# Kernel tuning notes

Hardware: AMD Instinct MI355X
Metric: run time of the kernel (lower is better)

The kernel has to match this reference:

```python
import jax, jax.numpy as jnp
import numpy as np

N = 50000      # nodes
E = 800000     # edges (before self-loops)
F_IN = 256     # nfeat
HEADS = 8      # nhead
C1 = 16        # hidden_sizes (per-head channels of conv1)
NCLS = 40      # nclass
NEG_SLOPE = 0.2


def setup_inputs() -> dict:
    key = jax.random.key(0)
    ks = jax.random.split(key, 12)
    s = 0.1
    x = jax.random.normal(ks[0], (N, F_IN), dtype=jnp.float32)
    edge_index = jax.random.randint(ks[1], (2, E), 0, N, dtype=jnp.int64)
    edge_attr = jax.random.normal(ks[2], (E,), dtype=jnp.float32)  # unused by forward
    W1 = jax.random.normal(ks[3], (F_IN, HEADS * C1), dtype=jnp.float32) * s
    att_src1 = jax.random.normal(ks[4], (HEADS, C1), dtype=jnp.float32) * s
    att_dst1 = jax.random.normal(ks[5], (HEADS, C1), dtype=jnp.float32) * s
    b1 = jnp.zeros((HEADS * C1,), dtype=jnp.float32)
    W2 = jax.random.normal(ks[6], (HEADS * C1, NCLS), dtype=jnp.float32) * s
    att_src2 = jax.random.normal(ks[7], (1, NCLS), dtype=jnp.float32) * s
    att_dst2 = jax.random.normal(ks[8], (1, NCLS), dtype=jnp.float32) * s
    b2 = jnp.zeros((NCLS,), dtype=jnp.float32)
    return {"x": x, "edge_index": edge_index, "edge_attr": edge_attr,
            "W1": W1, "att_src1": att_src1, "att_dst1": att_dst1, "b1": b1,
            "W2": W2, "att_src2": att_src2, "att_dst2": att_dst2, "b2": b2}


def gat_layer(x, W, att_src, att_dst, bias, src, dst, concat):
    """PyG-style GATConv (eval mode, no dropout). src/dst include self-loops."""
    H, C = att_src.shape
    h = (x @ W).reshape(-1, H, C)                     # [N,H,C]
    a_src = (h * att_src[None]).sum(-1)               # [N,H]
    a_dst = (h * att_dst[None]).sum(-1)               # [N,H]
    e = jax.nn.leaky_relu(a_src[src] + a_dst[dst], NEG_SLOPE)  # [Etot,H]
    # segment softmax over destination neighborhoods
    m = jax.ops.segment_max(e, dst, num_segments=N)   # [N,H]
    m = jax.lax.stop_gradient(jnp.where(jnp.isfinite(m), m, 0.0))
    p = jnp.exp(e - m[dst])
    denom = jax.ops.segment_sum(p, dst, num_segments=N)
    alpha = p / (denom[dst] + 1e-16)                  # [Etot,H]
    out = jax.ops.segment_sum(alpha[:, :, None] * h[src], dst, num_segments=N)  # [N,H,C]
    out = out.reshape(-1, H * C) if concat else out.mean(axis=1)
    return out + bias


def reference(x, edge_index, edge_attr, W1, att_src1, att_dst1, b1, W2, att_src2, att_dst2, b2):
    # add self loops (PyG GATConv default)
    loops = jnp.arange(N, dtype=edge_index.dtype)
    src = jnp.concatenate([edge_index[0], loops])
    dst = jnp.concatenate([edge_index[1], loops])
    # eval mode: F.dropout is identity
    h = jax.nn.elu(gat_layer(x, W1, att_src1, att_dst1, b1, src, dst, concat=True))
    final = gat_layer(h, W2, att_src2, att_dst2, b2, src, dst, concat=False)
    return final, jax.nn.log_softmax(final, axis=1)
```

## Files before the change

### kernel.cpp

```cpp
#include <hip/hip_runtime.h>

#define NN 50000
#define EE 800000
#define FIN 256
#define HD 8
#define C1 16
#define HC 128
#define NC 40
#define NEG 0.2f
#define CAP 64
#define BM 64
#define BM2 64
#define GB1 ((NN + BM - 1) / BM)
#define NP_N (NN / 8)
#define SCB 2048
#define PREPB 19

typedef __attribute__((ext_vector_type(8))) short short8;
typedef __attribute__((ext_vector_type(4))) float f32x4;
union FragU { uint4 u; short8 s; };

__device__ __forceinline__ float leaky(float v){ return v > 0.f ? v : NEG * v; }

__device__ __forceinline__ unsigned int f2bf(float f){
  unsigned int u = __float_as_uint(f);
  u += 0x7fffu + ((u >> 16) & 1u);
  return u >> 16;
}
__device__ __forceinline__ unsigned int pack2bf(float a, float b){
  return f2bf(a) | (f2bf(b) << 16);
}
__device__ __forceinline__ float bflo(unsigned int u){ return __uint_as_float(u << 16); }
__device__ __forceinline__ float bfhi(unsigned int u){ return __uint_as_float(u & 0xffff0000u); }
__device__ __forceinline__ float bfus(unsigned short u){ return __uint_as_float((unsigned int)u << 16); }

__device__ __forceinline__ void gld_lds16(const void* g, void* l){
  __builtin_amdgcn_global_load_lds((const __attribute__((address_space(1))) unsigned int*)g,
                                   (__attribute__((address_space(3))) unsigned int*)l,
                                   16, 0, 0);
}

__global__ __launch_bounds__(256) void k_prep(const float* __restrict__ W1,
                                              uint4* __restrict__ W1bfs,
                                              const float* __restrict__ W2,
                                              uint4* __restrict__ W2bfs,
                                              const int* __restrict__ ei,
                                              int* __restrict__ cnt,
                                              int* __restrict__ srcp){
  const int tid = threadIdx.x;
  if (blockIdx.x < 16){
    int f = blockIdx.x * 256 + tid;
    int lane = f & 63, nt = (f >> 6) & 7, kt = f >> 9;
    int quad = lane >> 4, l16 = lane & 15;
    const float* src = W1 + (size_t)(kt * 32 + quad * 8) * HC + nt * 16 + l16;
    unsigned int p[4];
#pragma unroll
    for (int jj = 0; jj < 4; jj++)
      p[jj] = pack2bf(src[(size_t)(2 * jj) * HC], src[(size_t)(2 * jj + 1) * HC]);
    W1bfs[f] = make_uint4(p[0], p[1], p[2], p[3]);
    return;
  }
  if (blockIdx.x < PREPB){
    int f = (blockIdx.x - 16) * 256 + tid;
    int lane = f & 63, frag = f >> 6;
    int kt = frag / 3, nt = frag - kt * 3;
    int quad = lane >> 4, l16 = lane & 15;
    int n = nt * 16 + l16;
    int k0 = kt * 32 + quad * 8;
    unsigned int p[4];
#pragma unroll
    for (int jj = 0; jj < 4; jj++){
      float v0 = (n < NC) ? W2[(size_t)(k0 + 2 * jj) * NC + n] : 0.f;
      float v1 = (n < NC) ? W2[(size_t)(k0 + 2 * jj + 1) * NC + n] : 0.f;
      p[jj] = pack2bf(v0, v1);
    }
    W2bfs[f] = make_uint4(p[0], p[1], p[2], p[3]);
    return;
  }
  const int b = blockIdx.x - PREPB;
  const int part = b & 7, rank = b >> 3;
  const int lo = part * NP_N, hi = lo + NP_N;
  for (int e = rank * 256 + tid; e < EE; e += 256 * 256){
    int d = ei[EE + e];
    if (d >= lo && d < hi){
      int s = ei[e];
      int pos = atomicAdd(&cnt[d], 1);
      if (pos < CAP) srcp[d * CAP + pos] = s;
    }
  }
}

__global__ __launch_bounds__(256, 2) void k_gemm1(const float* __restrict__ x,
                                                  const uint4* __restrict__ W1bfs,
                                                  const float* __restrict__ att_s,
                                                  const float* __restrict__ att_d,
                                                  unsigned short* __restrict__ h1b,
                                                  float* __restrict__ as1,
                                                  float* __restrict__ ad1){
  __shared__ float xs[BM * FIN];
  const int tid = threadIdx.x;
  const int wave = tid >> 6, lane = tid & 63;
  const int quad = lane >> 4, l16 = lane & 15;
  const int m0 = blockIdx.x * BM;
  const int wr0 = wave * 16;

#pragma unroll
  for (int i = 0; i < 16; i++){
    int grow = m0 + wr0 + i; if (grow >= NN) grow = NN - 1;
    const float* src = x + (size_t)grow * FIN + ((lane ^ (i & 7)) << 2);
    gld_lds16(src, &xs[(wr0 + i) * FIN]);
  }

  FragU bf[8];
#pragma unroll
  for (int nt = 0; nt < 8; nt++) bf[nt].u = W1bfs[nt * 64 + lane];

  asm volatile("s_waitcnt vmcnt(0)" ::: "memory");
  __builtin_amdgcn_sched_barrier(0);

  f32x4 acc[8];
#pragma unroll
  for (int t = 0; t < 8; t++) acc[t] = (f32x4){0.f, 0.f, 0.f, 0.f};

  const int swz = l16 & 7;
  const float* xrow = &xs[(wr0 + l16) * FIN];
#pragma unroll
  for (int kt = 0; kt < 8; kt++){
    FragU bn[8];
    if (kt < 7){
#pragma unroll
      for (int nt = 0; nt < 8; nt++)
        bn[nt].u = W1bfs[((kt + 1) * 8 + nt) * 64 + lane];
    }
    const int g0 = kt * 8 + quad * 2;
    const float4 a0 = *(const float4*)(xrow + ((g0 ^ swz) << 2));
    const float4 a1 = *(const float4*)(xrow + (((g0 + 1) ^ swz) << 2));
    FragU af;
    af.u = make_uint4(pack2bf(a0.x, a0.y), pack2bf(a0.z, a0.w),
                      pack2bf(a1.x, a1.y), pack2bf(a1.z, a1.w));
#pragma unroll
    for (int nt = 0; nt < 8; nt++)
      acc[nt] = __builtin_amdgcn_mfma_f32_16x16x32_bf16(af.s, bf[nt].s, acc[nt], 0, 0, 0);
    if (kt < 7){
#pragma unroll
      for (int nt = 0; nt < 8; nt++) bf[nt] = bn[nt];
    }
  }

  float sv[8], dv[8];
#pragma unroll
  for (int h = 0; h < 8; h++){ sv[h] = att_s[h * 16 + l16]; dv[h] = att_d[h * 16 + l16]; }
#pragma unroll
  for (int r = 0; r < 4; r++){
    const int gr = m0 + wr0 + quad * 4 + r;
    float s[8], d[8];
#pragma unroll
    for (int h = 0; h < 8; h++){ s[h] = acc[h][r] * sv[h]; d[h] = acc[h][r] * dv[h]; }
#pragma unroll
    for (int o = 1; o < 16; o <<= 1){
#pragma unroll
      for (int h = 0; h < 8; h++){ s[h] += __shfl_xor(s[h], o); d[h] += __shfl_xor(d[h], o); }
    }
    if (gr < NN){
#pragma unroll
      for (int h = 0; h < 8; h++)
        h1b[(size_t)gr * HC + h * 16 + l16] = (unsigned short)f2bf(acc[h][r]);
      if (l16 == 0){
        *(float4*)(as1 + gr * 8)     = make_float4(s[0], s[1], s[2], s[3]);
        *(float4*)(as1 + gr * 8 + 4) = make_float4(s[4], s[5], s[6], s[7]);
        *(float4*)(ad1 + gr * 8)     = make_float4(d[0], d[1], d[2], d[3]);
        *(float4*)(ad1 + gr * 8 + 4) = make_float4(d[4], d[5], d[6], d[7]);
      }
    }
  }
}

__global__ __launch_bounds__(512) void k_agg1(const int* __restrict__ srcp,
                                              const int* __restrict__ cnt,
                                              const float* __restrict__ as1,
                                              const float* __restrict__ ad1,
                                              const unsigned short* __restrict__ h1b,
                                              const float* __restrict__ b1,
                                              unsigned short* __restrict__ h2b){
  __shared__ float wls[8][64][8];
  __shared__ int   sls[8][64];
  const int lane = threadIdx.x & 63, w = threadIdx.x >> 6;
  const int n = blockIdx.x * 8 + w;
  int deg = cnt[n]; if (deg > CAP - 1) deg = CAP - 1;
  const int nE = deg + 1;
  int sA = n;
  if (lane < deg) sA = srcp[n * CAP + lane];
  sls[w][lane] = sA << 6;

  const int h = lane >> 3, e8 = lane & 7;
  const float adg = ad1[n * 8 + h];
  int nCh = (nE + 7) >> 3; if (nCh < 2) nCh = 2;

  float mx = -3.0e38f;
  for (int c = 0; c < nCh; c++){
    const int i = c * 8 + e8;
    const int s8 = sls[w][i] >> 3;
    const float v = (i < nE) ? leaky(as1[(size_t)(unsigned)(s8 + h)] + adg) : -3.0e38f;
    wls[w][i][h] = v;
    mx = fmaxf(mx, v);
  }
  mx = fmaxf(mx, __shfl_xor(mx, 1));
  mx = fmaxf(mx, __shfl_xor(mx, 2));
  mx = fmaxf(mx, __shfl_xor(mx, 4));

  float den = 0.f;
  for (int c = 0; c < nCh; c++){
    const int i = c * 8 + e8;
    const float v = wls[w][i][h];
    const float wt = (i < nE) ? __expf(v - mx) : 0.f;
    wls[w][i][h] = wt;
    den += wt;
  }
  den += __shfl_xor(den, 1);
  den += __shfl_xor(den, 2);
  den += __shfl_xor(den, 4);

  const unsigned int* hp = (const unsigned int*)h1b;
  float ax = 0.f, ay = 0.f;
  {
    unsigned int u[16]; float q[16];
#pragma unroll
    for (int i = 0; i < 16; i++){
      u[i] = hp[(size_t)(unsigned)(sls[w][i] + lane)];
      q[i] = wls[w][i][h];
    }
#pragma unroll
    for (int i = 0; i < 16; i++){ ax += q[i] * bflo(u[i]); ay += q[i] * bfhi(u[i]); }
  }
  for (int i0 = 16; i0 < nE; i0 += 8){
    unsigned int uu[8]; float qq[8];
#pragma unroll
    for (int t = 0; t < 8; t++){
      const int j = i0 + t;
      uu[t] = hp[(size_t)(unsigned)(sls[w][j] + lane)];
      qq[t] = (j < nE) ? wls[w][j][h] : 0.f;
    }
#pragma unroll
    for (int t = 0; t < 8; t++){ ax += qq[t] * bflo(uu[t]); ay += qq[t] * bfhi(uu[t]); }
  }

  const float invd = 1.f / (den + 1e-16f);
  const float2 bb = *(const float2*)(b1 + 2 * lane);
  float ox = ax * invd + bb.x;
  float oy = ay * invd + bb.y;
  ox = ox > 0.f ? ox : (__expf(ox) - 1.f);
  oy = oy > 0.f ? oy : (__expf(oy) - 1.f);
  *(unsigned int*)(h2b + (size_t)n * HC + 2 * lane) = pack2bf(ox, oy);
}

__global__ __launch_bounds__(256, 3) void k_gemm2(const unsigned short* __restrict__ h2b,
                                                  const uint4* __restrict__ W2bfs,
                                                  const float* __restrict__ att_s2,
                                                  const float* __restrict__ att_d2,
                                                  unsigned short* __restrict__ gb,
                                                  float* __restrict__ as2,
                                                  float* __restrict__ ad2){
  __shared__ unsigned short h2s[BM2 * HC];
  const int tid = threadIdx.x;
  const int wave = tid >> 6, lane = tid & 63;
  const int quad = lane >> 4, l16 = lane & 15;
  const int m0 = blockIdx.x * BM2;
  const int wr0 = wave * 16;

#pragma unroll
  for (int i = 0; i < 4; i++){
    const int rl = i * 4 + (lane >> 4);
    int grow = m0 + wr0 + rl; if (grow >= NN) grow = NN - 1;
    const int g = lane & 15;
    const unsigned short* src = h2b + (size_t)grow * HC + ((g ^ (rl & 7)) << 3);
    gld_lds16(src, &h2s[(wr0 + i * 4) * HC]);
  }

  FragU b2f[12];
#pragma unroll
  for (int f = 0; f < 12; f++) b2f[f].u = W2bfs[f * 64 + lane];

  asm volatile("s_waitcnt vmcnt(0)" ::: "memory");
  __builtin_amdgcn_sched_barrier(0);

  f32x4 acc[3];
#pragma unroll
  for (int t = 0; t < 3; t++) acc[t] = (f32x4){0.f, 0.f, 0.f, 0.f};

  const int swz = l16 & 7;
  const unsigned short* hrow = &h2s[(wr0 + l16) * HC];
#pragma unroll
  for (int kt = 0; kt < 4; kt++){
    FragU af;
    af.u = *(const uint4*)(hrow + (((kt * 4 + quad) ^ swz) << 3));
#pragma unroll
    for (int nt = 0; nt < 3; nt++)
      acc[nt] = __builtin_amdgcn_mfma_f32_16x16x32_bf16(af.s, b2f[kt * 3 + nt].s, acc[nt], 0, 0, 0);
  }

  float sv[3], dv[3];
#pragma unroll
  for (int nt = 0; nt < 3; nt++){
    const int c = nt * 16 + l16;
    sv[nt] = (c < NC) ? att_s2[c] : 0.f;
    dv[nt] = (c < NC) ? att_d2[c] : 0.f;
  }
#pragma unroll
  for (int r = 0; r < 4; r++){
    const int gr = m0 + wr0 + quad * 4 + r;
    float s = acc[0][r] * sv[0] + acc[1][r] * sv[1] + acc[2][r] * sv[2];
    float d = acc[0][r] * dv[0] + acc[1][r] * dv[1] + acc[2][r] * dv[2];
#pragma unroll
    for (int o = 1; o < 16; o <<= 1){ s += __shfl_xor(s, o); d += __shfl_xor(d, o); }
    if (gr < NN){
#pragma unroll
      for (int nt = 0; nt < 3; nt++){
        const int c = nt * 16 + l16;
        if (c < NC) gb[(size_t)gr * NC + c] = (unsigned short)f2bf(acc[nt][r]);
      }
      if (l16 == 0){ as2[gr] = s; ad2[gr] = d; }
    }
  }
}

__global__ __launch_bounds__(512) void k_agg2(const int* __restrict__ srcp,
                                              const int* __restrict__ cnt,
                                              const float* __restrict__ as2,
                                              const float* __restrict__ ad2,
                                              const unsigned short* __restrict__ gb,
                                              const float* __restrict__ b2,
                                              float* __restrict__ out){
  __shared__ float wls[8][64];
  __shared__ int   sls[8][64];
  const int lane = threadIdx.x & 63, w = threadIdx.x >> 6;
  const int n = blockIdx.x * 8 + w;
  int deg = cnt[n]; if (deg > CAP - 1) deg = CAP - 1;
  const int nE = deg + 1;
  const bool act = (lane <= deg);
  int sA = n;
  if (lane < deg) sA = srcp[n * CAP + lane];
  const float ad = ad2[n];
  float v = act ? leaky(as2[sA] + ad) : -3.0e38f;
  sls[w][lane] = sA * NC;
  float mx = v;
#pragma unroll
  for (int o = 1; o < 64; o <<= 1) mx = fmaxf(mx, __shfl_xor(mx, o));
  float wt = act ? __expf(v - mx) : 0.f;
  float den = wt;
#pragma unroll
  for (int o = 1; o < 64; o <<= 1) den += __shfl_xor(den, o);
  wls[w][lane] = wt;

  const int c = min(lane, NC - 1);
  float acc = 0.f;
  {
    float g[16], q[16];
#pragma unroll
    for (int i = 0; i < 16; i++){
      g[i] = bfus(gb[(size_t)(unsigned)(sls[w][i] + c)]);
      q[i] = wls[w][i];
    }
#pragma unroll
    for (int i = 0; i < 16; i++) acc += q[i] * g[i];
  }
  for (int i0 = 16; i0 < nE; i0 += 8){
    float gg[8], qq[8];
#pragma unroll
    for (int t = 0; t < 8; t++){
      const int j = i0 + t;
      gg[t] = bfus(gb[(size_t)(unsigned)(sls[w][j] + c)]);
      qq[t] = wls[w][j];
    }
#pragma unroll
    for (int t = 0; t < 8; t++) acc += qq[t] * gg[t];
  }
  const float invd = 1.f / (den + 1e-16f);
  const bool cl = (lane < NC);
  float f = acc * invd + b2[c];
  if (cl) out[(size_t)n * NC + lane] = f;
  float fv = cl ? f : -3.4e38f;
  float m2 = fv;
#pragma unroll
  for (int o = 1; o < 64; o <<= 1) m2 = fmaxf(m2, __shfl_xor(m2, o));
  float ex = cl ? __expf(fv - m2) : 0.f;
#pragma unroll
  for (int o = 1; o < 64; o <<= 1) ex += __shfl_xor(ex, o);
  const float lse = m2 + __logf(ex);
  if (cl) out[(size_t)(NN * NC) + (size_t)n * NC + lane] = fv - lse;
}

extern "C" void kernel_launch(void* const* d_in, const int* in_sizes, int n_in,
                              void* d_out, int out_size, void* d_ws, size_t ws_size,
                              hipStream_t stream){
  const float* x      = (const float*)d_in[0];
  const int*   ei     = (const int*)  d_in[1];
  const float* W1     = (const float*)d_in[3];
  const float* att_s1 = (const float*)d_in[4];
  const float* att_d1 = (const float*)d_in[5];
  const float* b1     = (const float*)d_in[6];
  const float* W2     = (const float*)d_in[7];
  const float* att_s2 = (const float*)d_in[8];
  const float* att_d2 = (const float*)d_in[9];
  const float* b2     = (const float*)d_in[10];
  float* out = (float*)d_out;

  char* wp = (char*)d_ws;
  uint4* W1bfs = (uint4*)wp;                 wp += (size_t)4096 * 16;
  uint4* W2bfs = (uint4*)wp;                 wp += (size_t)768 * 16;
  unsigned short* h1b = (unsigned short*)wp; wp += (size_t)NN * HC * 2;
  unsigned short* h2b = (unsigned short*)wp; wp += (size_t)NN * HC * 2;
  unsigned short* gb  = (unsigned short*)wp; wp += (size_t)NN * NC * 2;
  float* as1 = (float*)wp;                   wp += (size_t)NN * HD * 4;
  float* ad1 = (float*)wp;                   wp += (size_t)NN * HD * 4;
  float* as2 = (float*)wp;                   wp += (size_t)NN * 4;
  float* ad2 = (float*)wp;                   wp += (size_t)NN * 4;
  int* cnt   = (int*)wp;                     wp += (size_t)NN * 4;
  int* srcp  = (int*)wp;                     wp += (size_t)NN * CAP * 4;

  hipMemsetAsync(cnt, 0, (size_t)NN * sizeof(int), stream);
  k_prep  <<<PREPB + SCB, 256, 0, stream>>>(W1, W1bfs, W2, W2bfs, ei, cnt, srcp);
  k_gemm1 <<<GB1, 256, 0, stream>>>(x, W1bfs, att_s1, att_d1, h1b, as1, ad1);
  k_agg1  <<<NN / 8, 512, 0, stream>>>(srcp, cnt, as1, ad1, h1b, b1, h2b);
  k_gemm2 <<<(NN + BM2 - 1) / BM2, 256, 0, stream>>>(h2b, W2bfs, att_s2, att_d2, gb, as2, ad2);
  k_agg2  <<<NN / 8, 512, 0, stream>>>(srcp, cnt, as2, ad2, gb, b2, out);
}
```

Before: 238.2 us.

## Pre-convert x to bf16 in prep and process two nodes per wave in agg1

Adds blocks to the prep kernel that convert x to bf16 into workspace, so the first GEMM loads half-width rows into LDS and can run at higher occupancy. A fallback fp32 GEMM is kept for when the workspace is too small. The layer-1 aggregation now handles two destination nodes per wave with 32 lanes each loading 4 channels. This adds an extra full pass over x (read fp32, write bf16), and wave-level loops follow the larger of the two degrees.

```diff
diff --git a/kernel.cpp b/kernel.cpp
--- a/kernel.cpp
+++ b/kernel.cpp
@@ -15,6 +15,7 @@
 #define NP_N (NN / 8)
 #define SCB 2048
 #define PREPB 19
+#define CONVB 1024
 
 typedef __attribute__((ext_vector_type(8))) short short8;
 typedef __attribute__((ext_vector_type(4))) float f32x4;
@@ -44,6 +45,9 @@
                                               uint4* __restrict__ W1bfs,
                                               const float* __restrict__ W2,
                                               uint4* __restrict__ W2bfs,
+                                              const float* __restrict__ x,
+                                              uint4* __restrict__ xb,
+                                              int convb,
                                               const int* __restrict__ ei,
                                               int* __restrict__ cnt,
                                               int* __restrict__ srcp){
@@ -77,7 +81,18 @@
     W2bfs[f] = make_uint4(p[0], p[1], p[2], p[3]);
     return;
   }
-  const int b = blockIdx.x - PREPB;
+  if (blockIdx.x < PREPB + convb){
+    const int cb = blockIdx.x - PREPB;
+    const int stride = convb * 256;
+    for (int idx = cb * 256 + tid; idx < NN * FIN / 8; idx += stride){
+      const float4 v0 = *(const float4*)(x + (size_t)idx * 8);
+      const float4 v1 = *(const float4*)(x + (size_t)idx * 8 + 4);
+      xb[idx] = make_uint4(pack2bf(v0.x, v0.y), pack2bf(v0.z, v0.w),
+                           pack2bf(v1.x, v1.y), pack2bf(v1.z, v1.w));
+    }
+    return;
+  }
+  const int b = blockIdx.x - PREPB - convb;
   const int part = b & 7, rank = b >> 3;
   const int lo = part * NP_N, hi = lo + NP_N;
   for (int e = rank * 256 + tid; e < EE; e += 256 * 256){
@@ -90,14 +105,14 @@
   }
 }
 
-__global__ __launch_bounds__(256, 2) void k_gemm1(const float* __restrict__ x,
-                                                  const uint4* __restrict__ W1bfs,
-                                                  const float* __restrict__ att_s,
-                                                  const float* __restrict__ att_d,
-                                                  unsigned short* __restrict__ h1b,
-                                                  float* __restrict__ as1,
-                                                  float* __restrict__ ad1){
-  __shared__ float xs[BM * FIN];
+__global__ __launch_bounds__(256, 4) void k_gemm1b(const unsigned short* __restrict__ xb,
+                                                   const uint4* __restrict__ W1bfs,
+                                                   const float* __restrict__ att_s,
+                                                   const float* __restrict__ att_d,
+                                                   unsigned short* __restrict__ h1b,
+                                                   float* __restrict__ as1,
+                                                   float* __restrict__ ad1){
+  __shared__ unsigned short xs[BM * FIN];
   const int tid = threadIdx.x;
   const int wave = tid >> 6, lane = tid & 63;
   const int quad = lane >> 4, l16 = lane & 15;
@@ -105,10 +120,12 @@
   const int wr0 = wave * 16;
 
 #pragma unroll
-  for (int i = 0; i < 16; i++){
-    int grow = m0 + wr0 + i; if (grow >= NN) grow = NN - 1;
-    const float* src = x + (size_t)grow * FIN + ((lane ^ (i & 7)) << 2);
-    gld_lds16(src, &xs[(wr0 + i) * FIN]);
+  for (int i = 0; i < 8; i++){
+    const int rl = wr0 + i * 2 + (lane >> 5);
+    int grow = m0 + rl; if (grow >= NN) grow = NN - 1;
+    const int g = lane & 31;
+    const unsigned short* src = xb + (size_t)grow * FIN + ((g ^ (rl & 7)) << 3);
+    gld_lds16(src, &xs[(wr0 + i * 2) * FIN]);
   }
 
   FragU bf[8];
@@ -123,7 +140,7 @@
   for (int t = 0; t < 8; t++) acc[t] = (f32x4){0.f, 0.f, 0.f, 0.f};
 
   const int swz = l16 & 7;
-  const float* xrow = &xs[(wr0 + l16) * FIN];
+  const unsigned short* xrow = &xs[(wr0 + l16) * FIN];
 #pragma unroll
   for (int kt = 0; kt < 8; kt++){
     FragU bn[8];
@@ -132,12 +149,8 @@
       for (int nt = 0; nt < 8; nt++)
         bn[nt].u = W1bfs[((kt + 1) * 8 + nt) * 64 + lane];
     }
-    const int g0 = kt * 8 + quad * 2;
-    const float4 a0 = *(const float4*)(xrow + ((g0 ^ swz) << 2));
-    const float4 a1 = *(const float4*)(xrow + (((g0 + 1) ^ swz) << 2));
     FragU af;
-    af.u = make_uint4(pack2bf(a0.x, a0.y), pack2bf(a0.z, a0.w),
-                      pack2bf(a1.x, a1.y), pack2bf(a1.z, a1.w));
+    af.u = *(const uint4*)(xrow + (((kt * 4 + quad) ^ swz) << 3));
 #pragma unroll
     for (int nt = 0; nt < 8; nt++)
       acc[nt] = __builtin_amdgcn_mfma_f32_16x16x32_bf16(af.s, bf[nt].s, acc[nt], 0, 0, 0);
@@ -175,82 +188,187 @@
   }
 }
 
-__global__ __launch_bounds__(512) void k_agg1(const int* __restrict__ srcp,
+__global__ __launch_bounds__(256, 2) void k_gemm1f(const float* __restrict__ x,
+                                                   const uint4* __restrict__ W1bfs,
+                                                   const float* __restrict__ att_s,
+                                                   const float* __restrict__ att_d,
+                                                   unsigned short* __restrict__ h1b,
+                                                   float* __restrict__ as1,
+                                                   float* __restrict__ ad1){
+  __shared__ float xs[BM * FIN];
+  const int tid = threadIdx.x;
+  const int wave = tid >> 6, lane = tid & 63;
+  const int quad = lane >> 4, l16 = lane & 15;
+  const int m0 = blockIdx.x * BM;
+  const int wr0 = wave * 16;
+#pragma unroll
+  for (int i = 0; i < 16; i++){
+    int grow = m0 + wr0 + i; if (grow >= NN) grow = NN - 1;
+    const float* src = x + (size_t)grow * FIN + ((lane ^ (i & 7)) << 2);
+    gld_lds16(src, &xs[(wr0 + i) * FIN]);
+  }
+  FragU bf[8];
+#pragma unroll
+  for (int nt = 0; nt < 8; nt++) bf[nt].u = W1bfs[nt * 64 + lane];
+  asm volatile("s_waitcnt vmcnt(0)" ::: "memory");
+  __builtin_amdgcn_sched_barrier(0);
+  f32x4 acc[8];
+#pragma unroll
+  for (int t = 0; t < 8; t++) acc[t] = (f32x4){0.f, 0.f, 0.f, 0.f};
+  const int swz = l16 & 7;
+  const float* xrow = &xs[(wr0 + l16) * FIN];
+#pragma unroll
+  for (int kt = 0; kt < 8; kt++){
+    FragU bn[8];
+    if (kt < 7){
+#pragma unroll
+      for (int nt = 0; nt < 8; nt++)
+        bn[nt].u = W1bfs[((kt + 1) * 8 + nt) * 64 + lane];
+    }
+    const int g0 = kt * 8 + quad * 2;
+    const float4 a0 = *(const float4*)(xrow + ((g0 ^ swz) << 2));
+    const float4 a1 = *(const float4*)(xrow + (((g0 + 1) ^ swz) << 2));
+    FragU af;
+    af.u = make_uint4(pack2bf(a0.x, a0.y), pack2bf(a0.z, a0.w),
+                      pack2bf(a1.x, a1.y), pack2bf(a1.z, a1.w));
+#pragma unroll
+    for (int nt = 0; nt < 8; nt++)
+      acc[nt] = __builtin_amdgcn_mfma_f32_16x16x32_bf16(af.s, bf[nt].s, acc[nt], 0, 0, 0);
+    if (kt < 7){
+#pragma unroll
+      for (int nt = 0; nt < 8; nt++) bf[nt] = bn[nt];
+    }
+  }
+  float sv[8], dv[8];
+#pragma unroll
+  for (int h = 0; h < 8; h++){ sv[h] = att_s[h * 16 + l16]; dv[h] = att_d[h * 16 + l16]; }
+#pragma unroll
+  for (int r = 0; r < 4; r++){
+    const int gr = m0 + wr0 + quad * 4 + r;
+    float s[8], d[8];
+#pragma unroll
+    for (int h = 0; h < 8; h++){ s[h] = acc[h][r] * sv[h]; d[h] = acc[h][r] * dv[h]; }
+#pragma unroll
+    for (int o = 1; o < 16; o <<= 1){
+#pragma unroll
+      for (int h = 0; h < 8; h++){ s[h] += __shfl_xor(s[h], o); d[h] += __shfl_xor(d[h], o); }
+    }
+    if (gr < NN){
+#pragma unroll
+      for (int h = 0; h < 8; h++)
+        h1b[(size_t)gr * HC + h * 16 + l16] = (unsigned short)f2bf(acc[h][r]);
+      if (l16 == 0){
+        *(float4*)(as1 + gr * 8)     = make_float4(s[0], s[1], s[2], s[3]);
+        *(float4*)(as1 + gr * 8 + 4) = make_float4(s[4], s[5], s[6], s[7]);
+        *(float4*)(ad1 + gr * 8)     = make_float4(d[0], d[1], d[2], d[3]);
+        *(float4*)(ad1 + gr * 8 + 4) = make_float4(d[4], d[5], d[6], d[7]);
+      }
+    }
+  }
+}
+
+__global__ __launch_bounds__(256) void k_agg1(const int* __restrict__ srcp,
                                               const int* __restrict__ cnt,
                                               const float* __restrict__ as1,
                                               const float* __restrict__ ad1,
                                               const unsigned short* __restrict__ h1b,
                                               const float* __restrict__ b1,
                                               unsigned short* __restrict__ h2b){
-  __shared__ float wls[8][64][8];
-  __shared__ int   sls[8][64];
+  __shared__ float wls[4][2][64][8];
+  __shared__ int   sls[4][2][64];
+  __shared__ float dls[4][2][8];
   const int lane = threadIdx.x & 63, w = threadIdx.x >> 6;
-  const int n = blockIdx.x * 8 + w;
-  int deg = cnt[n]; if (deg > CAP - 1) deg = CAP - 1;
-  const int nE = deg + 1;
-  int sA = n;
-  if (lane < deg) sA = srcp[n * CAP + lane];
-  sls[w][lane] = sA << 6;
-
+  const int nb = blockIdx.x * 8 + w * 2;
   const int h = lane >> 3, e8 = lane & 7;
-  const float adg = ad1[n * 8 + h];
-  int nCh = (nE + 7) >> 3; if (nCh < 2) nCh = 2;
-
-  float mx = -3.0e38f;
-  for (int c = 0; c < nCh; c++){
-    const int i = c * 8 + e8;
-    const int s8 = sls[w][i] >> 3;
-    const float v = (i < nE) ? leaky(as1[(size_t)(unsigned)(s8 + h)] + adg) : -3.0e38f;
-    wls[w][i][h] = v;
-    mx = fmaxf(mx, v);
-  }
-  mx = fmaxf(mx, __shfl_xor(mx, 1));
-  mx = fmaxf(mx, __shfl_xor(mx, 2));
-  mx = fmaxf(mx, __shfl_xor(mx, 4));
-
-  float den = 0.f;
-  for (int c = 0; c < nCh; c++){
-    const int i = c * 8 + e8;
-    const float v = wls[w][i][h];
-    const float wt = (i < nE) ? __expf(v - mx) : 0.f;
-    wls[w][i][h] = wt;
-    den += wt;
-  }
-  den += __shfl_xor(den, 1);
-  den += __shfl_xor(den, 2);
-  den += __shfl_xor(den, 4);
-
-  const unsigned int* hp = (const unsigned int*)h1b;
-  float ax = 0.f, ay = 0.f;
+
+  int degs[2], nEs[2];
+#pragma unroll
+  for (int j = 0; j < 2; j++){
+    int d = cnt[nb + j]; if (d > CAP - 1) d = CAP - 1;
+    degs[j] = d; nEs[j] = d + 1;
+  }
+  const int nEm = max(nEs[0], nEs[1]);
+  int nCh = (nEm + 7) >> 3; if (nCh < 2) nCh = 2;
+
+#pragma unroll
+  for (int j = 0; j < 2; j++){
+    const int n = nb + j;
+    const int deg = degs[j], nE = nEs[j];
+    int sA = n;
+    if (lane < deg) sA = srcp[n * CAP + lane];
+    sls[w][j][lane] = sA << 5;
+
+    const float adg = ad1[n * 8 + h];
+    float mx = -3.0e38f;
+    for (int c = 0; c < nCh; c++){
+      const int i = c * 8 + e8;
+      const int s8 = sls[w][j][i] >> 2;
+      const float v = (i < nE) ? leaky(as1[(size_t)(unsigned)(s8 + h)] + adg) : -3.0e38f;
+      wls[w][j][i][h] = v;
+      mx = fmaxf(mx, v);
+    }
+    mx = fmaxf(mx, __shfl_xor(mx, 1));
+    mx = fmaxf(mx, __shfl_xor(mx, 2));
+    mx = fmaxf(mx, __shfl_xor(mx, 4));
+
+    float den = 0.f;
+    for (int c = 0; c < nCh; c++){
+      const int i = c * 8 + e8;
+      const float v = wls[w][j][i][h];
+      const float wt = (i < nE) ? __expf(v - mx) : 0.f;
+      wls[w][j][i][h] = wt;
+      den += wt;
+    }
+    den += __shfl_xor(den, 1);
+    den += __shfl_xor(den, 2);
+    den += __shfl_xor(den, 4);
+    if (e8 == 0) dls[w][j][h] = den;
+  }
+
+  const int j = lane >> 5, l32 = lane & 31, hb = l32 >> 2;
+  const uint2* hp = (const uint2*)h1b;
+  float a0 = 0.f, a1 = 0.f, a2 = 0.f, a3 = 0.f;
   {
-    unsigned int u[16]; float q[16];
+    uint2 u[16]; float q[16];
 #pragma unroll
     for (int i = 0; i < 16; i++){
-      u[i] = hp[(size_t)(unsigned)(sls[w][i] + lane)];
-      q[i] = wls[w][i][h];
-    }
-#pragma unroll
-    for (int i = 0; i < 16; i++){ ax += q[i] * bflo(u[i]); ay += q[i] * bfhi(u[i]); }
-  }
-  for (int i0 = 16; i0 < nE; i0 += 8){
-    unsigned int uu[8]; float qq[8];
+      u[i] = hp[(size_t)(unsigned)(sls[w][j][i] + l32)];
+      q[i] = wls[w][j][i][hb];
+    }
+#pragma unroll
+    for (int i = 0; i < 16; i++){
+      a0 += q[i] * bflo(u[i].x); a1 += q[i] * bfhi(u[i].x);
+      a2 += q[i] * bflo(u[i].y); a3 += q[i] * bfhi(u[i].y);
+    }
+  }
+  for (int i0 = 16; i0 < nEm; i0 += 8){
+    uint2 uu[8]; float qq[8];
 #pragma unroll
     for (int t = 0; t < 8; t++){
-      const int j = i0 + t;
-      uu[t] = hp[(size_t)(unsigned)(sls[w][j] + lane)];
-      qq[t] = (j < nE) ? wls[w][j][h] : 0.f;
-    }
-#pragma unroll
-    for (int t = 0; t < 8; t++){ ax += qq[t] * bflo(uu[t]); ay += qq[t] * bfhi(uu[t]); }
-  }
-
-  const float invd = 1.f / (den + 1e-16f);
-  const float2 bb = *(const float2*)(b1 + 2 * lane);
-  float ox = ax * invd + bb.x;
-  float oy = ay * invd + bb.y;
-  ox = ox > 0.f ? ox : (__expf(ox) - 1.f);
-  oy = oy > 0.f ? oy : (__expf(oy) - 1.f);
-  *(unsigned int*)(h2b + (size_t)n * HC + 2 * lane) = pack2bf(ox, oy);
+      const int i = i0 + t;
+      uu[t] = hp[(size_t)(unsigned)(sls[w][j][i] + l32)];
+      qq[t] = wls[w][j][i][hb];
+    }
+#pragma unroll
+    for (int t = 0; t < 8; t++){
+      a0 += qq[t] * bflo(uu[t].x); a1 += qq[t] * bfhi(uu[t].x);
+      a2 += qq[t] * bflo(uu[t].y); a3 += qq[t] * bfhi(uu[t].y);
+    }
+  }
+
+  const int n = nb + j;
+  const float invd = 1.f / (dls[w][j][hb] + 1e-16f);
+  const float4 bb = *(const float4*)(b1 + 4 * l32);
+  float o0 = a0 * invd + bb.x;
+  float o1 = a1 * invd + bb.y;
+  float o2 = a2 * invd + bb.z;
+  float o3 = a3 * invd + bb.w;
+  o0 = o0 > 0.f ? o0 : (__expf(o0) - 1.f);
+  o1 = o1 > 0.f ? o1 : (__expf(o1) - 1.f);
+  o2 = o2 > 0.f ? o2 : (__expf(o2) - 1.f);
+  o3 = o3 > 0.f ? o3 : (__expf(o3) - 1.f);
+  uint2 pk; pk.x = pack2bf(o0, o1); pk.y = pack2bf(o2, o3);
+  ((uint2*)h2b)[(size_t)n * 32 + l32] = pk;
 }
 
 __global__ __launch_bounds__(256, 3) void k_gemm2(const unsigned short* __restrict__ h2b,
@@ -416,11 +534,20 @@
   float* ad2 = (float*)wp;                   wp += (size_t)NN * 4;
   int* cnt   = (int*)wp;                     wp += (size_t)NN * 4;
   int* srcp  = (int*)wp;                     wp += (size_t)NN * CAP * 4;
+  uint4* xb  = (uint4*)wp;                   wp += (size_t)NN * FIN * 2;
+
+  const bool usebf = ws_size >= (size_t)(wp - (char*)d_ws);
+  const int convb = usebf ? CONVB : 0;
 
   hipMemsetAsync(cnt, 0, (size_t)NN * sizeof(int), stream);
-  k_prep  <<<PREPB + SCB, 256, 0, stream>>>(W1, W1bfs, W2, W2bfs, ei, cnt, srcp);
-  k_gemm1 <<<GB1, 256, 0, stream>>>(x, W1bfs, att_s1, att_d1, h1b, as1, ad1);
-  k_agg1  <<<NN / 8, 512, 0, stream>>>(srcp, cnt, as1, ad1, h1b, b1, h2b);
+  k_prep <<<PREPB + convb + SCB, 256, 0, stream>>>(W1, W1bfs, W2, W2bfs, x, xb, convb,
+                                                   ei, cnt, srcp);
+  if (usebf)
+    k_gemm1b <<<GB1, 256, 0, stream>>>((const unsigned short*)xb, W1bfs, att_s1, att_d1,
+                                       h1b, as1, ad1);
+  else
+    k_gemm1f <<<GB1, 256, 0, stream>>>(x, W1bfs, att_s1, att_d1, h1b, as1, ad1);
+  k_agg1  <<<NN / 8, 256, 0, stream>>>(srcp, cnt, as1, ad1, h1b, b1, h2b);
   k_gemm2 <<<(NN + BM2 - 1) / BM2, 256, 0, stream>>>(h2b, W2bfs, att_s2, att_d2, gb, as2, ad2);
   k_agg2  <<<NN / 8, 512, 0, stream>>>(srcp, cnt, as2, ad2, gb, b2, out);
 }
```

Result: no change. 240.4 us (+0.9%).

## Process two nodes per wave in agg1 with 8-byte gathers; vectorize edge scatter

Applied to the files above, without the earlier changes.

The first-layer aggregation now has each 64-lane wave handle two destination nodes. Each half-wave gathers 8-byte rows (four bf16 channels per lane) instead of 4-byte pairs, and the block shrinks to 256 threads. This is meant to halve the number of waves and use wider memory transactions for the neighbour feature gather. The cost is that each wave loops to the larger of the two node degrees, so some lanes idle. Separately, the edge-scatter prep blocks are moved to the front of the grid and read destination indices two at a time as int2.

```diff
diff --git a/kernel.cpp b/kernel.cpp
--- a/kernel.cpp
+++ b/kernel.cpp
@@ -48,8 +48,28 @@
                                               int* __restrict__ cnt,
                                               int* __restrict__ srcp){
   const int tid = threadIdx.x;
-  if (blockIdx.x < 16){
-    int f = blockIdx.x * 256 + tid;
+  if (blockIdx.x < SCB){
+    const int part = blockIdx.x & 7, rank = blockIdx.x >> 3;
+    const int lo = part * NP_N, hi = lo + NP_N;
+    const int2* dp = (const int2*)(ei + EE);
+    for (int e2 = rank * 256 + tid; e2 < EE / 2; e2 += 256 * 256){
+      const int2 d2 = dp[e2];
+      if (d2.x >= lo && d2.x < hi){
+        int s = ei[2 * e2];
+        int pos = atomicAdd(&cnt[d2.x], 1);
+        if (pos < CAP) srcp[d2.x * CAP + pos] = s;
+      }
+      if (d2.y >= lo && d2.y < hi){
+        int s = ei[2 * e2 + 1];
+        int pos = atomicAdd(&cnt[d2.y], 1);
+        if (pos < CAP) srcp[d2.y * CAP + pos] = s;
+      }
+    }
+    return;
+  }
+  const int pb = blockIdx.x - SCB;
+  if (pb < 16){
+    int f = pb * 256 + tid;
     int lane = f & 63, nt = (f >> 6) & 7, kt = f >> 9;
     int quad = lane >> 4, l16 = lane & 15;
     const float* src = W1 + (size_t)(kt * 32 + quad * 8) * HC + nt * 16 + l16;
@@ -60,34 +80,20 @@
     W1bfs[f] = make_uint4(p[0], p[1], p[2], p[3]);
     return;
   }
-  if (blockIdx.x < PREPB){
-    int f = (blockIdx.x - 16) * 256 + tid;
-    int lane = f & 63, frag = f >> 6;
-    int kt = frag / 3, nt = frag - kt * 3;
-    int quad = lane >> 4, l16 = lane & 15;
-    int n = nt * 16 + l16;
-    int k0 = kt * 32 + quad * 8;
-    unsigned int p[4];
-#pragma unroll
-    for (int jj = 0; jj < 4; jj++){
-      float v0 = (n < NC) ? W2[(size_t)(k0 + 2 * jj) * NC + n] : 0.f;
-      float v1 = (n < NC) ? W2[(size_t)(k0 + 2 * jj + 1) * NC + n] : 0.f;
-      p[jj] = pack2bf(v0, v1);
-    }
-    W2bfs[f] = make_uint4(p[0], p[1], p[2], p[3]);
-    return;
-  }
-  const int b = blockIdx.x - PREPB;
-  const int part = b & 7, rank = b >> 3;
-  const int lo = part * NP_N, hi = lo + NP_N;
-  for (int e = rank * 256 + tid; e < EE; e += 256 * 256){
-    int d = ei[EE + e];
-    if (d >= lo && d < hi){
-      int s = ei[e];
-      int pos = atomicAdd(&cnt[d], 1);
-      if (pos < CAP) srcp[d * CAP + pos] = s;
-    }
-  }
+  int f = (pb - 16) * 256 + tid;
+  int lane = f & 63, frag = f >> 6;
+  int kt = frag / 3, nt = frag - kt * 3;
+  int quad = lane >> 4, l16 = lane & 15;
+  int n = nt * 16 + l16;
+  int k0 = kt * 32 + quad * 8;
+  unsigned int p[4];
+#pragma unroll
+  for (int jj = 0; jj < 4; jj++){
+    float v0 = (n < NC) ? W2[(size_t)(k0 + 2 * jj) * NC + n] : 0.f;
+    float v1 = (n < NC) ? W2[(size_t)(k0 + 2 * jj + 1) * NC + n] : 0.f;
+    p[jj] = pack2bf(v0, v1);
+  }
+  W2bfs[f] = make_uint4(p[0], p[1], p[2], p[3]);
 }
 
 __global__ __launch_bounds__(256, 2) void k_gemm1(const float* __restrict__ x,
@@ -175,82 +181,108 @@
   }
 }
 
-__global__ __launch_bounds__(512) void k_agg1(const int* __restrict__ srcp,
+__global__ __launch_bounds__(256) void k_agg1(const int* __restrict__ srcp,
                                               const int* __restrict__ cnt,
                                               const float* __restrict__ as1,
                                               const float* __restrict__ ad1,
                                               const unsigned short* __restrict__ h1b,
                                               const float* __restrict__ b1,
                                               unsigned short* __restrict__ h2b){
-  __shared__ float wls[8][64][8];
-  __shared__ int   sls[8][64];
+  __shared__ float wls[4][2][64][8];
+  __shared__ int   sls[4][2][64];
+  __shared__ float dls[4][2][8];
   const int lane = threadIdx.x & 63, w = threadIdx.x >> 6;
-  const int n = blockIdx.x * 8 + w;
-  int deg = cnt[n]; if (deg > CAP - 1) deg = CAP - 1;
-  const int nE = deg + 1;
-  int sA = n;
-  if (lane < deg) sA = srcp[n * CAP + lane];
-  sls[w][lane] = sA << 6;
-
+  const int nb = blockIdx.x * 8 + w * 2;
   const int h = lane >> 3, e8 = lane & 7;
-  const float adg = ad1[n * 8 + h];
-  int nCh = (nE + 7) >> 3; if (nCh < 2) nCh = 2;
-
-  float mx = -3.0e38f;
-  for (int c = 0; c < nCh; c++){
-    const int i = c * 8 + e8;
-    const int s8 = sls[w][i] >> 3;
-    const float v = (i < nE) ? leaky(as1[(size_t)(unsigned)(s8 + h)] + adg) : -3.0e38f;
-    wls[w][i][h] = v;
-    mx = fmaxf(mx, v);
-  }
-  mx = fmaxf(mx, __shfl_xor(mx, 1));
-  mx = fmaxf(mx, __shfl_xor(mx, 2));
-  mx = fmaxf(mx, __shfl_xor(mx, 4));
-
-  float den = 0.f;
-  for (int c = 0; c < nCh; c++){
-    const int i = c * 8 + e8;
-    const float v = wls[w][i][h];
-    const float wt = (i < nE) ? __expf(v - mx) : 0.f;
-    wls[w][i][h] = wt;
-    den += wt;
-  }
-  den += __shfl_xor(den, 1);
-  den += __shfl_xor(den, 2);
-  den += __shfl_xor(den, 4);
-
-  const unsigned int* hp = (const unsigned int*)h1b;
-  float ax = 0.f, ay = 0.f;
+
+  int degs[2], nEs[2];
+#pragma unroll
+  for (int j = 0; j < 2; j++){
+    int d = cnt[nb + j]; if (d > CAP - 1) d = CAP - 1;
+    degs[j] = d; nEs[j] = d + 1;
+  }
+  const int nEm = max(nEs[0], nEs[1]);
+  int nCh = (nEm + 7) >> 3; if (nCh < 2) nCh = 2;
+
+#pragma unroll
+  for (int j = 0; j < 2; j++){
+    const int n = nb + j;
+    const int deg = degs[j], nE = nEs[j];
+    int sA = n;
+    if (lane < deg) sA = srcp[n * CAP + lane];
+    sls[w][j][lane] = sA << 5;
+
+    const float adg = ad1[n * 8 + h];
+    float mx = -3.0e38f;
+    for (int c = 0; c < nCh; c++){
+      const int i = c * 8 + e8;
+      const int s8 = sls[w][j][i] >> 2;
+      const float v = (i < nE) ? leaky(as1[(size_t)(unsigned)(s8 + h)] + adg) : -3.0e38f;
+      wls[w][j][i][h] = v;
+      mx = fmaxf(mx, v);
+    }
+    mx = fmaxf(mx, __shfl_xor(mx, 1));
+    mx = fmaxf(mx, __shfl_xor(mx, 2));
+    mx = fmaxf(mx, __shfl_xor(mx, 4));
+
+    float den = 0.f;
+    for (int c = 0; c < nCh; c++){
+      const int i = c * 8 + e8;
+      const float v = wls[w][j][i][h];
+      const float wt = (i < nE) ? __expf(v - mx) : 0.f;
+      wls[w][j][i][h] = wt;
+      den += wt;
+    }
+    den += __shfl_xor(den, 1);
+    den += __shfl_xor(den, 2);
+    den += __shfl_xor(den, 4);
+    if (e8 == 0) dls[w][j][h] = den;
+  }
+
+  const int j = lane >> 5, l32 = lane & 31, hb = l32 >> 2;
+  const uint2* hp = (const uint2*)h1b;
+  float a0 = 0.f, a1 = 0.f, a2 = 0.f, a3 = 0.f;
   {
-    unsigned int u[16]; float q[16];
+    uint2 u[16]; float q[16];
 #pragma unroll
     for (int i = 0; i < 16; i++){
-      u[i] = hp[(size_t)(unsigned)(sls[w][i] + lane)];
-      q[i] = wls[w][i][h];
-    }
-#pragma unroll
-    for (int i = 0; i < 16; i++){ ax += q[i] * bflo(u[i]); ay += q[i] * bfhi(u[i]); }
-  }
-  for (int i0 = 16; i0 < nE; i0 += 8){
-    unsigned int uu[8]; float qq[8];
+      u[i] = hp[(size_t)(unsigned)(sls[w][j][i] + l32)];
+      q[i] = wls[w][j][i][hb];
+    }
+#pragma unroll
+    for (int i = 0; i < 16; i++){
+      a0 += q[i] * bflo(u[i].x); a1 += q[i] * bfhi(u[i].x);
+      a2 += q[i] * bflo(u[i].y); a3 += q[i] * bfhi(u[i].y);
+    }
+  }
+  for (int i0 = 16; i0 < nEm; i0 += 8){
+    uint2 uu[8]; float qq[8];
 #pragma unroll
     for (int t = 0; t < 8; t++){
-      const int j = i0 + t;
-      uu[t] = hp[(size_t)(unsigned)(sls[w][j] + lane)];
-      qq[t] = (j < nE) ? wls[w][j][h] : 0.f;
-    }
-#pragma unroll
-    for (int t = 0; t < 8; t++){ ax += qq[t] * bflo(uu[t]); ay += qq[t] * bfhi(uu[t]); }
-  }
-
-  const float invd = 1.f / (den + 1e-16f);
-  const float2 bb = *(const float2*)(b1 + 2 * lane);
-  float ox = ax * invd + bb.x;
-  float oy = ay * invd + bb.y;
-  ox = ox > 0.f ? ox : (__expf(ox) - 1.f);
-  oy = oy > 0.f ? oy : (__expf(oy) - 1.f);
-  *(unsigned int*)(h2b + (size_t)n * HC + 2 * lane) = pack2bf(ox, oy);
+      const int i = i0 + t;
+      uu[t] = hp[(size_t)(unsigned)(sls[w][j][i] + l32)];
+      qq[t] = wls[w][j][i][hb];
+    }
+#pragma unroll
+    for (int t = 0; t < 8; t++){
+      a0 += qq[t] * bflo(uu[t].x); a1 += qq[t] * bfhi(uu[t].x);
+      a2 += qq[t] * bflo(uu[t].y); a3 += qq[t] * bfhi(uu[t].y);
+    }
+  }
+
+  const int n = nb + j;
+  const float invd = 1.f / (dls[w][j][hb] + 1e-16f);
+  const float4 bb = *(const float4*)(b1 + 4 * l32);
+  float o0 = a0 * invd + bb.x;
+  float o1 = a1 * invd + bb.y;
+  float o2 = a2 * invd + bb.z;
+  float o3 = a3 * invd + bb.w;
+  o0 = o0 > 0.f ? o0 : (__expf(o0) - 1.f);
+  o1 = o1 > 0.f ? o1 : (__expf(o1) - 1.f);
+  o2 = o2 > 0.f ? o2 : (__expf(o2) - 1.f);
+  o3 = o3 > 0.f ? o3 : (__expf(o3) - 1.f);
+  uint2 pk; pk.x = pack2bf(o0, o1); pk.y = pack2bf(o2, o3);
+  ((uint2*)h2b)[(size_t)n * 32 + l32] = pk;
 }
 
 __global__ __launch_bounds__(256, 3) void k_gemm2(const unsigned short* __restrict__ h2b,
@@ -418,9 +450,9 @@
   int* srcp  = (int*)wp;                     wp += (size_t)NN * CAP * 4;
 
   hipMemsetAsync(cnt, 0, (size_t)NN * sizeof(int), stream);
-  k_prep  <<<PREPB + SCB, 256, 0, stream>>>(W1, W1bfs, W2, W2bfs, ei, cnt, srcp);
+  k_prep  <<<SCB + PREPB, 256, 0, stream>>>(W1, W1bfs, W2, W2bfs, ei, cnt, srcp);
   k_gemm1 <<<GB1, 256, 0, stream>>>(x, W1bfs, att_s1, att_d1, h1b, as1, ad1);
-  k_agg1  <<<NN / 8, 512, 0, stream>>>(srcp, cnt, as1, ad1, h1b, b1, h2b);
+  k_agg1  <<<NN / 8, 256, 0, stream>>>(srcp, cnt, as1, ad1, h1b, b1, h2b);
   k_gemm2 <<<(NN + BM2 - 1) / BM2, 256, 0, stream>>>(h2b, W2bfs, att_s2, att_d2, gb, as2, ad2);
   k_agg2  <<<NN / 8, 512, 0, stream>>>(srcp, cnt, as2, ad2, gb, b2, out);
 }
```

After: 235.7 us. About the same (-1.1%).
